# Kernel tuning notes

Measured on AMD Instinct MI355X. Metric: run time of the kernel, lower is better.

The kernel has to match this reference:

```python
import jax, jax.numpy as jnp
import numpy as np

N = 50000      # nodes
E = 400000     # edges
D = 128        # node / hidden dim
DE = 64        # edge feature dim
Z = 2 * D + DE # CGConv concat dim


def setup_inputs() -> dict:
    key = jax.random.key(0)
    ks = jax.random.split(key, 12)
    s = 0.05
    return {
        "x": jax.random.normal(ks[0], (N, D), jnp.float32),
        "edge_index": jax.random.randint(ks[1], (2, E), 0, N, jnp.int64),
        "edge_attr": jax.random.normal(ks[2], (E, DE), jnp.float32),
        # conv1 params (lin_f: gate, lin_s: core), z-dim -> D
        "Wf1": jax.random.normal(ks[3], (Z, D), jnp.float32) * s,
        "bf1": jnp.zeros((D,), jnp.float32),
        "Ws1": jax.random.normal(ks[4], (Z, D), jnp.float32) * s,
        "bs1": jnp.zeros((D,), jnp.float32),
        # conv2 params
        "Wf2": jax.random.normal(ks[5], (Z, D), jnp.float32) * s,
        "bf2": jnp.zeros((D,), jnp.float32),
        "Ws2": jax.random.normal(ks[6], (Z, D), jnp.float32) * s,
        "bs2": jnp.zeros((D,), jnp.float32),
        # final linear D -> 1
        "Wfc": jax.random.normal(ks[7], (D, 1), jnp.float32) * s,
        "bfc": jnp.zeros((1,), jnp.float32),
    }


def _cgconv(h, edge_attr, src, dst, Wf, bf, Ws, bs):
    # PyG CGConv: z_ij = [x_i, x_j, e_ij]; out_i = x_i + sum_j sigmoid(lin_f(z)) * softplus(lin_s(z))
    # x_i = target = edge_index[1], x_j = source = edge_index[0]
    z = jnp.concatenate([h[dst], h[src], edge_attr], axis=-1)  # [E, Z]
    msg = jax.nn.sigmoid(z @ Wf + bf) * jax.nn.softplus(z @ Ws + bs)  # [E, D]
    agg = jax.ops.segment_sum(msg, dst, num_segments=h.shape[0])  # [N, D]
    return h + agg


def reference(x, edge_index, edge_attr, Wf1, bf1, Ws1, bs1, Wf2, bf2, Ws2, bs2, Wfc, bfc):
    src, dst = edge_index[0], edge_index[1]
    h = _cgconv(x, edge_attr, src, dst, Wf1, bf1, Ws1, bs1)
    h = jax.nn.relu(h)
    h = _cgconv(h, edge_attr, src, dst, Wf2, bf2, Ws2, bs2)
    return h @ Wfc + bfc  # [N, 1]
```

## Files before the change

### kernel.cpp

```cpp
#include <hip/hip_runtime.h>
#include <math.h>

#define NN 50000
#define NE 400000

typedef __attribute__((ext_vector_type(8))) short bf16x8;
typedef __attribute__((ext_vector_type(4))) float f32x4;
typedef unsigned short ushort_t;

__device__ __forceinline__ unsigned short f2bf(float f) {
    unsigned int u = __float_as_uint(f);
    u += 0x7FFF + ((u >> 16) & 1);
    return (unsigned short)(u >> 16);
}
__device__ __forceinline__ float2 upk(unsigned int w) {
    float2 r;
    r.x = __uint_as_float(w << 16);
    r.y = __uint_as_float(w & 0xFFFF0000u);
    return r;
}

#define LOG2E 1.4426950408889634f
#define LN2   0.6931471805599453f

__device__ __forceinline__ float msg_act(float gf, float gs) {
    float tf = __builtin_amdgcn_exp2f(gf * -LOG2E);
    float sig = __builtin_amdgcn_rcpf(1.0f + tf) * LN2;
    float ts = __builtin_amdgcn_exp2f(gs * LOG2E);
    float lg = __builtin_amdgcn_logf(1.0f + ts);
    return sig * lg;
}

__global__ void pack_weights(const float* __restrict__ Wf, const float* __restrict__ bf,
                             const float* __restrict__ Ws, const float* __restrict__ bs,
                             ushort_t* __restrict__ WT, ushort_t* __restrict__ WeT,
                             float* __restrict__ bcat) {
    int i = blockIdx.x * 256 + threadIdx.x;
    if (i < 512 * 128) {
        int c = i >> 7, k = i & 127;
        float w;
        if (c < 128)      w = Wf[k * 128 + c];
        else if (c < 256) w = Wf[(128 + k) * 128 + (c - 128)];
        else if (c < 384) w = Ws[k * 128 + (c - 256)];
        else              w = Ws[(128 + k) * 128 + (c - 384)];
        WT[i] = f2bf(w);
    } else if (i < 512 * 128 + 256 * 64) {
        int j = i - 512 * 128;
        int c = j >> 6, k = j & 63;
        float w = (c < 128) ? Wf[(256 + k) * 128 + c] : Ws[(256 + k) * 128 + (c - 128)];
        WeT[j] = f2bf(w);
    } else if (i < 512 * 128 + 256 * 64 + 256) {
        int c = i - (512 * 128 + 256 * 64);
        bcat[c] = (c < 128) ? bf[c] : bs[c - 128];
    }
}

__global__ void cvt_bf16(const float* __restrict__ in, ushort_t* __restrict__ out, int n8) {
    int i = blockIdx.x * 256 + threadIdx.x;
    if (i >= n8) return;
    const float4* p = (const float4*)in + (size_t)i * 2;
    float4 a = p[0], b = p[1];
    bf16x8 v;
    v[0] = (short)f2bf(a.x); v[1] = (short)f2bf(a.y);
    v[2] = (short)f2bf(a.z); v[3] = (short)f2bf(a.w);
    v[4] = (short)f2bf(b.x); v[5] = (short)f2bf(b.y);
    v[6] = (short)f2bf(b.z); v[7] = (short)f2bf(b.w);
    *((bf16x8*)out + i) = v;
}

__global__ __launch_bounds__(256) void node_gemm(const ushort_t* __restrict__ hb,
                                                 const ushort_t* __restrict__ WT,
                                                 ushort_t* __restrict__ P) {
    __shared__ ushort_t Bs[128 * 136];
    const int tid = threadIdx.x;
    const int w = tid >> 6, l = tid & 63;
    const int by = blockIdx.y;
    const ushort_t* src = WT + (size_t)by * 128 * 128;
    #pragma unroll
    for (int j = 0; j < 8; ++j) {
        int cid = j * 256 + tid;
        int row = cid >> 4, off = (cid & 15) * 8;
        *(bf16x8*)(&Bs[row * 136 + off]) = *(const bf16x8*)(src + row * 128 + off);
    }
    __syncthreads();
    const int r0 = blockIdx.x * 64 + w * 16;
    const int lrow = l & 15, lk = l >> 4;
    int arow = r0 + lrow;
    if (arow >= NN) arow = NN - 1;
    f32x4 acc[8];
    #pragma unroll
    for (int i = 0; i < 8; ++i) acc[i] = (f32x4){0.f, 0.f, 0.f, 0.f};
    #pragma unroll
    for (int ks = 0; ks < 4; ++ks) {
        int kb = ks * 32 + lk * 8;
        bf16x8 af = *(const bf16x8*)(hb + (size_t)arow * 128 + kb);
        #pragma unroll
        for (int nc = 0; nc < 8; ++nc) {
            bf16x8 bfr = *(const bf16x8*)(&Bs[(nc * 16 + lrow) * 136 + kb]);
            acc[nc] = __builtin_amdgcn_mfma_f32_16x16x32_bf16(af, bfr, acc[nc], 0, 0, 0);
        }
    }
    const int rb = r0 + lk * 4;
    const int cb = by * 128;
    #pragma unroll
    for (int nc = 0; nc < 8; ++nc) {
        int col = cb + nc * 16 + lrow;
        #pragma unroll
        for (int r = 0; r < 4; ++r) {
            int row = rb + r;
            if (row < NN) P[(size_t)row * 512 + col] = f2bf(acc[nc][r]);
        }
    }
}

__global__ __launch_bounds__(512, 2) void edge_fused(const int* __restrict__ ei,
                                                     const ushort_t* __restrict__ eab,
                                                     const ushort_t* __restrict__ WeT,
                                                     const float* __restrict__ bcat,
                                                     const ushort_t* __restrict__ P,
                                                     ushort_t* __restrict__ hacc) {
    __shared__ ushort_t Qs[64 * 264];
    const int tid = threadIdx.x;
    const int w = tid >> 6, l = tid & 63;
    const int lrow = l & 15, lk = l >> 4;
    const int e0 = blockIdx.x * 64;

    {
        const int tile = w >> 1, half = w & 1;
        f32x4 acc[8];
        #pragma unroll
        for (int i = 0; i < 8; ++i) acc[i] = (f32x4){0.f, 0.f, 0.f, 0.f};
        const int arow = e0 + tile * 16 + lrow;
        const ushort_t* wslice = WeT + (size_t)half * 128 * 64;
        #pragma unroll
        for (int ks = 0; ks < 2; ++ks) {
            int kb = ks * 32 + lk * 8;
            bf16x8 af = *(const bf16x8*)(eab + (size_t)arow * 64 + kb);
            #pragma unroll
            for (int nc = 0; nc < 8; ++nc) {
                bf16x8 bfr = *(const bf16x8*)(wslice + (size_t)(nc * 16 + lrow) * 64 + kb);
                acc[nc] = __builtin_amdgcn_mfma_f32_16x16x32_bf16(af, bfr, acc[nc], 0, 0, 0);
            }
        }
        #pragma unroll
        for (int nc = 0; nc < 8; ++nc) {
            int col = half * 128 + nc * 16 + lrow;
            float bb = bcat[col];
            #pragma unroll
            for (int r = 0; r < 4; ++r) {
                Qs[(tile * 16 + lk * 4 + r) * 264 + col] = f2bf(acc[nc][r] + bb);
            }
        }
    }
    __syncthreads();

    int dd[8];
    unsigned int A[8], B[8], C[8], D[8], QF[8], QS[8];
    #pragma unroll
    for (int i = 0; i < 8; ++i) {
        int j = w * 8 + i;
        int e = e0 + j;
        int s = ei[e];
        int d = ei[NE + e];
        dd[i] = d;
        const unsigned int* Pd = (const unsigned int*)(P + (size_t)d * 512);
        const unsigned int* Ps = (const unsigned int*)(P + (size_t)s * 512);
        A[i] = Pd[l];
        B[i] = Ps[64 + l];
        C[i] = Pd[128 + l];
        D[i] = Ps[192 + l];
        const unsigned int* qr = (const unsigned int*)(Qs + (size_t)j * 264);
        QF[i] = qr[l];
        QS[i] = qr[64 + l];
    }
    __builtin_amdgcn_sched_barrier(0);
    #pragma unroll
    for (int i = 0; i < 8; ++i) {
        float2 af_ = upk(A[i]);
        float2 bf_ = upk(B[i]);
        float2 as_ = upk(C[i]);
        float2 bs_ = upk(D[i]);
        float2 qf = upk(QF[i]);
        float2 qs = upk(QS[i]);
        float m0 = msg_act(af_.x + bf_.x + qf.x, as_.x + bs_.x + qs.x);
        float m1 = msg_act(af_.y + bf_.y + qf.y, as_.y + bs_.y + qs.y);
        unsigned int pk = (unsigned int)f2bf(m0) | ((unsigned int)f2bf(m1) << 16);
        unsigned int* addr = (unsigned int*)(hacc + (size_t)dd[i] * 128 + 2 * l);
        asm volatile("global_atomic_pk_add_bf16 %0, %1, off" :: "v"(addr), "v"(pk));
    }
}

__global__ void relu_bf(const ushort_t* __restrict__ in, ushort_t* __restrict__ out, int n8) {
    int i = blockIdx.x * 256 + threadIdx.x;
    if (i >= n8) return;
    uint4 v = ((const uint4*)in)[i];
    unsigned int* pv = (unsigned int*)&v;
    #pragma unroll
    for (int j = 0; j < 4; ++j) {
        unsigned int u = pv[j];
        unsigned int lo = (u & 0x8000u) ? 0u : (u & 0xFFFFu);
        unsigned int hi = (u & 0x80000000u) ? 0u : (u & 0xFFFF0000u);
        pv[j] = lo | hi;
    }
    ((uint4*)out)[i] = v;
}

__global__ __launch_bounds__(256) void final_fc(const ushort_t* __restrict__ hb,
                                                const float* __restrict__ W,
                                                const float* __restrict__ b,
                                                float* __restrict__ out) {
    int gid = blockIdx.x * 256 + threadIdx.x;
    int n = gid >> 6, lane = gid & 63;
    if (n >= NN) return;
    unsigned int hv = ((const unsigned int*)(hb + (size_t)n * 128))[lane];
    float2 h2 = upk(hv);
    float2 wv = ((const float2*)W)[lane];
    float p = h2.x * wv.x + h2.y * wv.y;
    #pragma unroll
    for (int off = 32; off > 0; off >>= 1) p += __shfl_down(p, off);
    if (lane == 0) out[n] = p + b[0];
}

extern "C" void kernel_launch(void* const* d_in, const int* in_sizes, int n_in,
                              void* d_out, int out_size, void* d_ws, size_t ws_size,
                              hipStream_t stream) {
    const float* x   = (const float*)d_in[0];
    const int*   ei  = (const int*)d_in[1];
    const float* ea  = (const float*)d_in[2];
    const float* Wf1 = (const float*)d_in[3];
    const float* bf1 = (const float*)d_in[4];
    const float* Ws1 = (const float*)d_in[5];
    const float* bs1 = (const float*)d_in[6];
    const float* Wf2 = (const float*)d_in[7];
    const float* bf2 = (const float*)d_in[8];
    const float* Ws2 = (const float*)d_in[9];
    const float* bs2 = (const float*)d_in[10];
    const float* Wfc = (const float*)d_in[11];
    const float* bfc = (const float*)d_in[12];
    float* out = (float*)d_out;

    ushort_t* hb1 = (ushort_t*)d_ws;
    ushort_t* hb2 = hb1 + (size_t)NN * 128;
    ushort_t* P   = hb2 + (size_t)NN * 128;
    ushort_t* eab = P + (size_t)NN * 512;
    ushort_t* WT  = eab + (size_t)NE * 64;
    ushort_t* WeT = WT + 2 * 512 * 128;
    float* bcat   = (float*)(WeT + 2 * 256 * 64);

    cvt_bf16<<<(NN * 128 / 8 + 255) / 256, 256, 0, stream>>>(x, hb1, NN * 128 / 8);
    cvt_bf16<<<(NE * 64 / 8 + 255) / 256, 256, 0, stream>>>(ea, eab, NE * 64 / 8);
    const int packN = 512 * 128 + 256 * 64 + 256;
    pack_weights<<<(packN + 255) / 256, 256, 0, stream>>>(Wf1, bf1, Ws1, bs1,
                                                          WT, WeT, bcat);
    pack_weights<<<(packN + 255) / 256, 256, 0, stream>>>(Wf2, bf2, Ws2, bs2,
                                                          WT + 512 * 128, WeT + 256 * 64, bcat + 256);

    for (int conv = 0; conv < 2; ++conv) {
        ushort_t* h = conv ? hb2 : hb1;
        node_gemm<<<dim3((NN + 63) / 64, 4), 256, 0, stream>>>(h, WT + conv * 512 * 128, P);
        edge_fused<<<NE / 64, 512, 0, stream>>>(ei, eab, WeT + conv * 256 * 64,
                                                bcat + conv * 256, P, h);
        if (conv == 0) {
            relu_bf<<<(NN * 128 / 8 + 255) / 256, 256, 0, stream>>>(hb1, hb2, NN * 128 / 8);
        }
    }
    final_fc<<<((size_t)NN * 64 + 255) / 256, 256, 0, stream>>>(hb2, Wfc, bfc, out);
}
```

Measured before the change: 371.0 us.

## Sort edges by destination and pre-reduce messages before atomics

Builds a counting-sort permutation of edges by destination node (histogram, single-block scan, scatter) and stores edge features in bf16 in sorted order. The edge kernel walks edges in that order, sums consecutive same-destination messages in registers, and issues one packed bf16 atomic per run instead of one per edge. It also remaps block IDs so that each XCD processes a contiguous range of edges. This aims to cut atomic traffic and improve locality, at the cost of several extra preprocessing kernels, including a serial single-block scan, run on every call.

```diff
diff --git a/kernel.cpp b/kernel.cpp
--- a/kernel.cpp
+++ b/kernel.cpp
@@ -29,6 +29,67 @@
     float ts = __builtin_amdgcn_exp2f(gs * LOG2E);
     float lg = __builtin_amdgcn_logf(1.0f + ts);
     return sig * lg;
+}
+
+__global__ void zero_cnt(int* __restrict__ cnt) {
+    int i = blockIdx.x * 256 + threadIdx.x;
+    if (i < NN) cnt[i] = 0;
+}
+__global__ void hist_k(const int* __restrict__ ei, int* __restrict__ cnt) {
+    int e = blockIdx.x * 256 + threadIdx.x;
+    if (e < NE) atomicAdd(&cnt[ei[NE + e]], 1);
+}
+__global__ __launch_bounds__(1024) void scan_k(const int* __restrict__ cnt,
+                                               int* __restrict__ off) {
+    __shared__ int part[1024];
+    const int t = threadIdx.x;
+    const int CH = (NN + 1023) / 1024;
+    const int s0 = t * CH;
+    int sum = 0;
+    for (int i = 0; i < CH; ++i) {
+        int idx = s0 + i;
+        if (idx < NN) sum += cnt[idx];
+    }
+    part[t] = sum;
+    __syncthreads();
+    for (int d = 1; d < 1024; d <<= 1) {
+        int v = (t >= d) ? part[t - d] : 0;
+        __syncthreads();
+        part[t] += v;
+        __syncthreads();
+    }
+    int run = t ? part[t - 1] : 0;
+    for (int i = 0; i < CH; ++i) {
+        int idx = s0 + i;
+        if (idx < NN) {
+            off[idx] = run;
+            run += cnt[idx];
+        }
+    }
+}
+__global__ void scatter_k(const int* __restrict__ ei, int* __restrict__ off,
+                          int* __restrict__ perm) {
+    int e = blockIdx.x * 256 + threadIdx.x;
+    if (e < NE) {
+        int d = ei[NE + e];
+        int pos = atomicAdd(&off[d], 1);
+        perm[pos] = e;
+    }
+}
+__global__ void permute_ea(const float* __restrict__ ea, const int* __restrict__ perm,
+                           ushort_t* __restrict__ out) {
+    int gid = blockIdx.x * 256 + threadIdx.x;
+    if (gid >= NE * 8) return;
+    int i = gid >> 3, part = gid & 7;
+    int p = perm[i];
+    const float4* src = (const float4*)(ea + (size_t)p * 64 + part * 8);
+    float4 a = src[0], b = src[1];
+    bf16x8 v;
+    v[0] = (short)f2bf(a.x); v[1] = (short)f2bf(a.y);
+    v[2] = (short)f2bf(a.z); v[3] = (short)f2bf(a.w);
+    v[4] = (short)f2bf(b.x); v[5] = (short)f2bf(b.y);
+    v[6] = (short)f2bf(b.z); v[7] = (short)f2bf(b.w);
+    *(bf16x8*)(out + (size_t)i * 64 + part * 8) = v;
 }
 
 __global__ void pack_weights(const float* __restrict__ Wf, const float* __restrict__ bf,
@@ -114,6 +175,7 @@
 }
 
 __global__ __launch_bounds__(512, 2) void edge_fused(const int* __restrict__ ei,
+                                                     const int* __restrict__ perm,
                                                      const ushort_t* __restrict__ eab,
                                                      const ushort_t* __restrict__ WeT,
                                                      const float* __restrict__ bcat,
@@ -123,7 +185,11 @@
     const int tid = threadIdx.x;
     const int w = tid >> 6, l = tid & 63;
     const int lrow = l & 15, lk = l >> 4;
-    const int e0 = blockIdx.x * 64;
+    const int nwg = gridDim.x;
+    const int q = nwg >> 3, r = nwg & 7;
+    const int xcd = blockIdx.x & 7, sub = blockIdx.x >> 3;
+    const int wgid = (xcd < r ? xcd * (q + 1) : r * (q + 1) + (xcd - r) * q) + sub;
+    const int e0 = wgid * 64;
 
     {
         const int tile = w >> 1, half = w & 1;
@@ -147,8 +213,8 @@
             int col = half * 128 + nc * 16 + lrow;
             float bb = bcat[col];
             #pragma unroll
-            for (int r = 0; r < 4; ++r) {
-                Qs[(tile * 16 + lk * 4 + r) * 264 + col] = f2bf(acc[nc][r] + bb);
+            for (int r2 = 0; r2 < 4; ++r2) {
+                Qs[(tile * 16 + lk * 4 + r2) * 264 + col] = f2bf(acc[nc][r2] + bb);
             }
         }
     }
@@ -159,9 +225,9 @@
     #pragma unroll
     for (int i = 0; i < 8; ++i) {
         int j = w * 8 + i;
-        int e = e0 + j;
-        int s = ei[e];
-        int d = ei[NE + e];
+        int p = perm[e0 + j];
+        int s = ei[p];
+        int d = ei[NE + p];
         dd[i] = d;
         const unsigned int* Pd = (const unsigned int*)(P + (size_t)d * 512);
         const unsigned int* Ps = (const unsigned int*)(P + (size_t)s * 512);
@@ -174,6 +240,7 @@
         QS[i] = qr[64 + l];
     }
     __builtin_amdgcn_sched_barrier(0);
+    float acc0 = 0.f, acc1 = 0.f;
     #pragma unroll
     for (int i = 0; i < 8; ++i) {
         float2 af_ = upk(A[i]);
@@ -182,11 +249,15 @@
         float2 bs_ = upk(D[i]);
         float2 qf = upk(QF[i]);
         float2 qs = upk(QS[i]);
-        float m0 = msg_act(af_.x + bf_.x + qf.x, as_.x + bs_.x + qs.x);
-        float m1 = msg_act(af_.y + bf_.y + qf.y, as_.y + bs_.y + qs.y);
-        unsigned int pk = (unsigned int)f2bf(m0) | ((unsigned int)f2bf(m1) << 16);
-        unsigned int* addr = (unsigned int*)(hacc + (size_t)dd[i] * 128 + 2 * l);
-        asm volatile("global_atomic_pk_add_bf16 %0, %1, off" :: "v"(addr), "v"(pk));
+        acc0 += msg_act(af_.x + bf_.x + qf.x, as_.x + bs_.x + qs.x);
+        acc1 += msg_act(af_.y + bf_.y + qf.y, as_.y + bs_.y + qs.y);
+        if (i == 7 || dd[i + 1] != dd[i]) {
+            unsigned int pk = (unsigned int)f2bf(acc0) | ((unsigned int)f2bf(acc1) << 16);
+            unsigned int* addr = (unsigned int*)(hacc + (size_t)dd[i] * 128 + 2 * l);
+            asm volatile("global_atomic_pk_add_bf16 %0, %1, off" :: "v"(addr), "v"(pk));
+            acc0 = 0.f;
+            acc1 = 0.f;
+        }
     }
 }
 
@@ -246,9 +317,17 @@
     ushort_t* WT  = eab + (size_t)NE * 64;
     ushort_t* WeT = WT + 2 * 512 * 128;
     float* bcat   = (float*)(WeT + 2 * 256 * 64);
+    int* cnt      = (int*)(bcat + 512);
+    int* off      = cnt + NN;
+    int* perm     = off + NN;
+
+    zero_cnt<<<(NN + 255) / 256, 256, 0, stream>>>(cnt);
+    hist_k<<<(NE + 255) / 256, 256, 0, stream>>>(ei, cnt);
+    scan_k<<<1, 1024, 0, stream>>>(cnt, off);
+    scatter_k<<<(NE + 255) / 256, 256, 0, stream>>>(ei, off, perm);
+    permute_ea<<<(NE * 8 + 255) / 256, 256, 0, stream>>>(ea, perm, eab);
 
     cvt_bf16<<<(NN * 128 / 8 + 255) / 256, 256, 0, stream>>>(x, hb1, NN * 128 / 8);
-    cvt_bf16<<<(NE * 64 / 8 + 255) / 256, 256, 0, stream>>>(ea, eab, NE * 64 / 8);
     const int packN = 512 * 128 + 256 * 64 + 256;
     pack_weights<<<(packN + 255) / 256, 256, 0, stream>>>(Wf1, bf1, Ws1, bs1,
                                                           WT, WeT, bcat);
@@ -258,7 +337,7 @@
     for (int conv = 0; conv < 2; ++conv) {
         ushort_t* h = conv ? hb2 : hb1;
         node_gemm<<<dim3((NN + 63) / 64, 4), 256, 0, stream>>>(h, WT + conv * 512 * 128, P);
-        edge_fused<<<NE / 64, 512, 0, stream>>>(ei, eab, WeT + conv * 256 * 64,
+        edge_fused<<<NE / 64, 512, 0, stream>>>(ei, perm, eab, WeT + conv * 256 * 64,
                                                 bcat + conv * 256, P, h);
         if (conv == 0) {
             relu_bf<<<(NN * 128 / 8 + 255) / 256, 256, 0, stream>>>(hb1, hb2, NN * 128 / 8);
```

New measurement: 485.3 us. 1.31x slower.
